# Performance work log

Measured on AMD Instinct MI355X. Metric: run time of the kernel, lower is better.

Reference implementation:

```python
import jax, jax.numpy as jnp
import numpy as np

B, T, M, P, F = 1024, 50, 128, 128, 64  # batch, timesteps, enc_hidden, dec_hidden, feat
BN_EPS = 1e-5


def setup_inputs() -> dict:
    key = jax.random.key(0)
    ks = jax.random.split(key, 20)
    s = 0.05
    inp = {
        "X_encoded": jax.random.normal(ks[0], (B, T, M), jnp.float32),
        "y_prev": jax.random.normal(ks[1], (B, T, F), jnp.float32),
        # attn_layer: Linear(2P+M -> M), Tanh, Linear(M -> 1)
        "attn_w1": jax.random.normal(ks[2], (M, 2 * P + M), jnp.float32) * s,
        "attn_b1": jnp.zeros((M,), jnp.float32),
        "attn_w2": jax.random.normal(ks[3], (1, M), jnp.float32) * s,
        "attn_b2": jnp.zeros((1,), jnp.float32),
        # fc: Linear(M+F -> F) + BatchNorm1d(F) (eval mode, running stats)
        "fc_w": jax.random.normal(ks[4], (F, M + F), jnp.float32) * s,
        "fc_b": jnp.zeros((F,), jnp.float32),
        "bn_gamma": jnp.ones((F,), jnp.float32),
        "bn_beta": jnp.zeros((F,), jnp.float32),
        "bn_mean": jnp.zeros((F,), jnp.float32),
        "bn_var": jnp.ones((F,), jnp.float32),
        # 2-layer LSTM (input F -> hidden P); gate order i,f,g,o as in torch
        "w_ih0": jax.random.normal(ks[5], (4 * P, F), jnp.float32) * s,
        "w_hh0": jax.random.normal(ks[6], (4 * P, P), jnp.float32) * s,
        "b_ih0": jnp.zeros((4 * P,), jnp.float32),
        "b_hh0": jnp.zeros((4 * P,), jnp.float32),
        "w_ih1": jax.random.normal(ks[7], (4 * P, P), jnp.float32) * s,
        "w_hh1": jax.random.normal(ks[8], (4 * P, P), jnp.float32) * s,
        "b_ih1": jnp.zeros((4 * P,), jnp.float32),
        "b_hh1": jnp.zeros((4 * P,), jnp.float32),
        # fc_final: Linear(P+M -> F) + ReLU
        "fcf_w": jax.random.normal(ks[9], (F, P + M), jnp.float32) * s,
        "fcf_b": jnp.zeros((F,), jnp.float32),
    }
    return inp


def _lstm_cell(x, h, c, w_ih, w_hh, b_ih, b_hh):
    g = x @ w_ih.T + b_ih + h @ w_hh.T + b_hh
    i, f, gg, o = jnp.split(g, 4, axis=-1)
    c2 = jax.nn.sigmoid(f) * c + jax.nn.sigmoid(i) * jnp.tanh(gg)
    h2 = jax.nn.sigmoid(o) * jnp.tanh(c2)
    return h2, c2


def reference(X_encoded, y_prev, attn_w1, attn_b1, attn_w2, attn_b2,
              fc_w, fc_b, bn_gamma, bn_beta, bn_mean, bn_var,
              w_ih0, w_hh0, b_ih0, b_hh0, w_ih1, w_hh1, b_ih1, b_hh1,
              fcf_w, fcf_b):
    b, t, m = X_encoded.shape
    p = w_hh0.shape[1]
    # split attn W1 over the concat [d_n[-1]; c_n[-1]; X_encoded]
    w1_d = attn_w1[:, :p]
    w1_c = attn_w1[:, p:2 * p]
    w1_x = attn_w1[:, 2 * p:]
    x_proj = jnp.einsum('btm,nm->btn', X_encoded, w1_x)  # [B,T,M], loop-invariant

    def step(carry, y_t):
        h0, c0, h1, c1, _ = carry
        state_proj = h1 @ w1_d.T + c1 @ w1_c.T + attn_b1          # [B,M]
        score = jnp.tanh(x_proj + state_proj[:, None, :]) @ attn_w2[0] + attn_b2[0]  # [B,T]
        beta = jax.nn.softmax(score, axis=1)
        context = jnp.einsum('bt,btm->bm', beta, X_encoded)        # [B,M]
        z = jnp.concatenate([context, y_t], axis=1) @ fc_w.T + fc_b
        y_tilde = (z - bn_mean) * jax.lax.rsqrt(bn_var + BN_EPS) * bn_gamma + bn_beta
        h0n, c0n = _lstm_cell(y_tilde, h0, c0, w_ih0, w_hh0, b_ih0, b_hh0)
        h1n, c1n = _lstm_cell(h0n, h1, c1, w_ih1, w_hh1, b_ih1, b_hh1)
        return (h0n, c0n, h1n, c1n, context), None

    zeros_p = jnp.zeros((b, p), X_encoded.dtype)
    zeros_m = jnp.zeros((b, m), X_encoded.dtype)
    init = (zeros_p, zeros_p, zeros_p, zeros_p, zeros_m)
    (h0, c0, h1, c1, context), _ = jax.lax.scan(init=init, f=step, xs=jnp.swapaxes(y_prev, 0, 1))
    y_pred = jax.nn.relu(jnp.concatenate([h1, context], axis=1) @ fcf_w.T + fcf_b)
    return y_pred
```

## Files before the change

kernel.cpp:

```cpp
#include <hip/hip_runtime.h>
#include <math.h>

#define TT 50
#define MM 128
#define PP 128
#define FF 64
#define NB 4
#define NTHR 512
#define BN_EPS 1e-5f

typedef unsigned int   u32;
typedef unsigned short u16;
typedef _Float16 f16x8 __attribute__((ext_vector_type(8)));
typedef float    f32x4 __attribute__((ext_vector_type(4)));

#define MFMA16(a, b, c) __builtin_amdgcn_mfma_f32_16x16x32_f16((a), (b), (c), 0, 0, 0)

__device__ __forceinline__ float fsig(float x)  { return 1.0f / (1.0f + __expf(-x)); }
__device__ __forceinline__ float ftanh(float x) { return 1.0f - 2.0f / (__expf(2.0f * x) + 1.0f); }
__device__ __forceinline__ u16 f2h(float x) { _Float16 h = (_Float16)x; u16 r; __builtin_memcpy(&r, &h, 2); return r; }
__device__ __forceinline__ float h2f(u16 u) { _Float16 h; __builtin_memcpy(&h, &u, 2); return (float)h; }

__device__ __forceinline__ void lds_barrier() {
    asm volatile("s_waitcnt lgkmcnt(0)\n\ts_barrier" ::: "memory");
}

__global__ __launch_bounds__(256) void packA_k(const float* __restrict__ w1, u16* __restrict__ dst) {
    int i = blockIdx.x * 256 + threadIdx.x;
    if (i >= 8 * 8 * 64 * 8) return;
    int j = i & 7, l = (i >> 3) & 63, ks = (i >> 9) & 7, tile = i >> 12;
    int row = tile * 16 + (l & 15);
    int k = ks * 32 + ((l >> 4) & 3) * 8 + j;
    dst[i] = f2h(w1[row * 384 + k]);
}
__global__ __launch_bounds__(256) void packE_k(const float* __restrict__ fcw, u16* __restrict__ dst) {
    int i = blockIdx.x * 256 + threadIdx.x;
    if (i >= 4 * 6 * 64 * 8) return;
    int j = i & 7, l = (i >> 3) & 63, r = i >> 9;
    int ks = r % 6, tile = r / 6;
    int row = tile * 16 + (l & 15);
    int k = ks * 32 + ((l >> 4) & 3) * 8 + j;
    dst[i] = f2h(fcw[row * 192 + k]);
}
__global__ __launch_bounds__(256) void packF_k(const float* __restrict__ wih0, const float* __restrict__ whh0,
                                               u16* __restrict__ dst) {
    int i = blockIdx.x * 256 + threadIdx.x;
    if (i >= 8 * 24 * 64 * 8) return;
    int j = i & 7, l = (i >> 3) & 63, rem = i >> 9;
    int wv = rem / 24, t = rem % 24, ks = t >> 2, g = t & 3;
    int row = g * 128 + wv * 16 + (l & 15);
    int k = ks * 32 + ((l >> 4) & 3) * 8 + j;
    float v = (k < 64) ? wih0[row * 64 + k] : whh0[row * 128 + (k - 64)];
    dst[i] = f2h(v);
}
__global__ __launch_bounds__(256) void packG_k(const float* __restrict__ wih1, const float* __restrict__ whh1,
                                               u16* __restrict__ dst) {
    int i = blockIdx.x * 256 + threadIdx.x;
    if (i >= 8 * 32 * 64 * 8) return;
    int j = i & 7, l = (i >> 3) & 63, rem = i >> 9;
    int wv = rem >> 5, t = rem & 31, ks = t >> 2, g = t & 3;
    int row = g * 128 + wv * 16 + (l & 15);
    int k = ks * 32 + ((l >> 4) & 3) * 8 + j;
    float v = (k < 128) ? wih1[row * 128 + k] : whh1[row * 128 + (k - 128)];
    dst[i] = f2h(v);
}

__global__ __launch_bounds__(NTHR, 2) void decoder_kernel(
    const float* __restrict__ X,
    const float* __restrict__ yprev,
    const float* __restrict__ w1,
    const float* __restrict__ b1,
    const float* __restrict__ w2,
    const float* __restrict__ b2,
    const float* __restrict__ fcb,
    const float* __restrict__ bng,
    const float* __restrict__ bnb,
    const float* __restrict__ bnm,
    const float* __restrict__ bnv,
    const float* __restrict__ bih0,
    const float* __restrict__ bhh0,
    const float* __restrict__ bih1,
    const float* __restrict__ bhh1,
    const float* __restrict__ fcfw,
    const float* __restrict__ fcfb,
    const u16* __restrict__ pA,
    const u16* __restrict__ pE,
    const u16* __restrict__ pF,
    const u16* __restrict__ pG,
    float* __restrict__ out)
{
    __shared__ __align__(16) u16   Xh[NB][TT][136];
    __shared__ __align__(16) u16   xph[NB][TT][140];
    __shared__ __align__(16) u16   h0h[2][NB][144];
    __shared__ __align__(16) u16   h1h[2][NB][144];
    __shared__ __align__(16) u16   c1h[NB][144];
    __shared__ __align__(16) u16   ytilh[NB][72];
    __shared__ __align__(16) u16   ctyh[NB][200];
    __shared__ __align__(16) float spf[NB][132];
    __shared__ __align__(16) float c0f[NB][132], c1f[NB][132];
    __shared__ __align__(16) float scs[NB][68];
    __shared__ __align__(16) float b1s[128], w2s[128];
    __shared__ __align__(16) float fck0s[FF], fck1s[FF];
    __shared__ __align__(16) float bsum0s[512], bsum1s[512];

    const int tid = threadIdx.x;
    const int b0 = blockIdx.x * NB;
    const int wv = tid >> 6, l = tid & 63;
    const int kg = (l >> 4) & 3;
    const int c4 = l & 3;
    const int cown = l & 15;

    for (int i4 = tid; i4 < NB * TT * 32; i4 += NTHR) {
        int bb = i4 / (TT * 32);
        int r  = i4 % (TT * 32);
        float4 v = ((const float4*)(X + (size_t)(b0 + bb) * TT * MM))[r];
        uint2 pk;
        pk.x = (u32)f2h(v.x) | ((u32)f2h(v.y) << 16);
        pk.y = (u32)f2h(v.z) | ((u32)f2h(v.w) << 16);
        *(uint2*)&Xh[bb][r >> 5][(r & 31) * 4] = pk;
    }
    for (int i = tid; i < NB * 144; i += NTHR) {
        int bb = i / 144, k = i % 144;
        h0h[0][bb][k] = 0; h0h[1][bb][k] = 0;
        h1h[0][bb][k] = 0; h1h[1][bb][k] = 0;
        c1h[bb][k] = 0;
        if (k < 132) { c0f[bb][k] = 0.f; c1f[bb][k] = 0.f; }
    }
    if (tid < 128) { b1s[tid] = b1[tid]; w2s[tid] = w2[tid]; }
    else if (tid < 192) {
        int f = tid - 128;
        float k1 = rsqrtf(bnv[f] + BN_EPS) * bng[f];
        fck1s[f] = k1;
        fck0s[f] = (fcb[f] - bnm[f]) * k1 + bnb[f];
    }
    bsum0s[tid] = bih0[tid] + bhh0[tid];
    bsum1s[tid] = bih1[tid] + bhh1[tid];

    const int bq = tid >> 7, rr = tid & 127;
    const bool own = rr < 2 * TT;
    const int tq = rr >> 1, qq = rr & 1;
    const float b2v = b2[0];

    if (own) {
        float xf[64];
        #pragma unroll
        for (int n = 0; n < 64; ++n) xf[n] = 0.f;
        const float* Xrow = X + ((size_t)(b0 + bq) * TT + tq) * MM;
        for (int m4 = 0; m4 < 32; ++m4) {
            float4 xv = *(const float4*)(Xrow + m4 * 4);
            #pragma unroll
            for (int n = 0; n < 64; ++n) {
                float4 w = *(const float4*)(w1 + (size_t)(qq * 64 + n) * 384 + 256 + m4 * 4);
                xf[n] += xv.x * w.x + xv.y * w.y + xv.z * w.z + xv.w * w.w;
            }
        }
        #pragma unroll
        for (int j = 0; j < 32; ++j) {
            u32 pk = (u32)f2h(xf[2 * j]) | ((u32)f2h(xf[2 * j + 1]) << 16);
            *(u32*)&xph[bq][tq][qq * 64 + 2 * j] = pk;
        }
    }
    __syncthreads();

    for (int ts = 0; ts < TT; ++ts) {
        const int p = ts & 1;

        {
            f32x4 acc = *(const f32x4*)&b1s[wv * 16 + kg * 4];
            const u16* abase = pA + (size_t)(wv * 8) * 512 + (size_t)l * 8;
            #pragma unroll
            for (int ks = 0; ks < 8; ++ks) {
                f16x8 a = *(const f16x8*)(abase + ks * 512);
                const u16* bp = (ks < 4) ? &h1h[p][c4][ks * 32 + kg * 8]
                                         : &c1h[c4][(ks - 4) * 32 + kg * 8];
                acc = MFMA16(a, *(const f16x8*)bp, acc);
            }
            if (cown < 4) *(f32x4*)&spf[cown][wv * 16 + kg * 4] = acc;
        }
        f16x8 ew[6];
        if (wv < 4) {
            const u16* abase = pE + (size_t)(wv * 6) * 512 + (size_t)l * 8;
            #pragma unroll
            for (int ks = 0; ks < 6; ++ks) ew[ks] = *(const f16x8*)(abase + ks * 512);
        }
        lds_barrier();

        if (own) {
            float acc = 0.f;
            #pragma unroll
            for (int jb = 0; jb < 8; ++jb) {
                int n = qq * 64 + jb * 8;
                uint4 xv  = *(const uint4*)&xph[bq][tq][n];
                f32x4 sp0 = *(const f32x4*)&spf[bq][n];
                f32x4 sp1 = *(const f32x4*)&spf[bq][n + 4];
                f32x4 wv0 = *(const f32x4*)&w2s[n];
                f32x4 wv1 = *(const f32x4*)&w2s[n + 4];
                acc += ftanh(h2f((u16)(xv.x & 0xffffu)) + sp0[0]) * wv0[0];
                acc += ftanh(h2f((u16)(xv.x >> 16))     + sp0[1]) * wv0[1];
                acc += ftanh(h2f((u16)(xv.y & 0xffffu)) + sp0[2]) * wv0[2];
                acc += ftanh(h2f((u16)(xv.y >> 16))     + sp0[3]) * wv0[3];
                acc += ftanh(h2f((u16)(xv.z & 0xffffu)) + sp1[0]) * wv1[0];
                acc += ftanh(h2f((u16)(xv.z >> 16))     + sp1[1]) * wv1[1];
                acc += ftanh(h2f((u16)(xv.w & 0xffffu)) + sp1[2]) * wv1[2];
                acc += ftanh(h2f((u16)(xv.w >> 16))     + sp1[3]) * wv1[3];
            }
            acc += __shfl_xor(acc, 1);
            if (qq == 0) scs[bq][tq] = acc + b2v;
        }
        lds_barrier();

        if (tid < 256) {
            int b = tid >> 6, t = tid & 63;
            float v = (t < TT) ? scs[b][t] : -1e30f;
            float mx = v;
            #pragma unroll
            for (int o = 32; o; o >>= 1) mx = fmaxf(mx, __shfl_xor(mx, o));
            float e = (t < TT) ? __expf(v - mx) : 0.f;
            float s = e;
            #pragma unroll
            for (int o = 32; o; o >>= 1) s += __shfl_xor(s, o);
            if (t < TT) scs[b][t] = e / s;
        } else {
            int i = tid - 256; int bb = i >> 6, f = i & 63;
            ctyh[bb][128 + f] = f2h(yprev[((size_t)(b0 + bb) * TT + ts) * FF + f]);
        }
        lds_barrier();

        f16x8 fw0[8];
        {
            const u16* pw = pF + (size_t)wv * 24 * 512 + (size_t)l * 8;
            #pragma unroll
            for (int q = 0; q < 8; ++q) fw0[q] = *(const f16x8*)(pw + q * 512);
        }
        {
            int bb = tid >> 7, m = tid & 127;
            float acc = 0.f;
            #pragma unroll 10
            for (int t = 0; t < TT; ++t) acc += scs[bb][t] * h2f(Xh[bb][t][m]);
            ctyh[bb][m] = f2h(acc);
        }
        lds_barrier();

        if (wv < 4) {
            f32x4 acc = {0.f, 0.f, 0.f, 0.f};
            #pragma unroll
            for (int ks = 0; ks < 6; ++ks) {
                f16x8 b = *(const f16x8*)&ctyh[c4][ks * 32 + kg * 8];
                acc = MFMA16(ew[ks], b, acc);
            }
            if (cown < 4) {
                int row = wv * 16 + kg * 4;
                f32x4 k1 = *(const f32x4*)&fck1s[row];
                f32x4 k0 = *(const f32x4*)&fck0s[row];
                #pragma unroll
                for (int r = 0; r < 4; ++r)
                    ytilh[cown][row + r] = f2h(acc[r] * k1[r] + k0[r]);
            }
        }
        lds_barrier();

        f16x8 gw0[8];
        {
            const u16* pw = pF + (size_t)wv * 24 * 512 + (size_t)l * 8;
            f32x4 a0 = *(const f32x4*)&bsum0s[0 * 128 + wv * 16 + kg * 4];
            f32x4 a1 = *(const f32x4*)&bsum0s[1 * 128 + wv * 16 + kg * 4];
            f32x4 a2 = *(const f32x4*)&bsum0s[2 * 128 + wv * 16 + kg * 4];
            f32x4 a3 = *(const f32x4*)&bsum0s[3 * 128 + wv * 16 + kg * 4];
            #pragma unroll
            for (int ks = 0; ks < 2; ++ks) {
                f16x8 b = *(const f16x8*)&ytilh[c4][ks * 32 + kg * 8];
                a0 = MFMA16(fw0[ks * 4 + 0], b, a0);
                a1 = MFMA16(fw0[ks * 4 + 1], b, a1);
                a2 = MFMA16(fw0[ks * 4 + 2], b, a2);
                a3 = MFMA16(fw0[ks * 4 + 3], b, a3);
            }
            #pragma unroll
            for (int ks = 2; ks < 6; ++ks) {
                f16x8 b = *(const f16x8*)&h0h[p][c4][(ks - 2) * 32 + kg * 8];
                a0 = MFMA16(*(const f16x8*)(pw + (ks * 4 + 0) * 512), b, a0);
                a1 = MFMA16(*(const f16x8*)(pw + (ks * 4 + 1) * 512), b, a1);
                a2 = MFMA16(*(const f16x8*)(pw + (ks * 4 + 2) * 512), b, a2);
                a3 = MFMA16(*(const f16x8*)(pw + (ks * 4 + 3) * 512), b, a3);
            }
            {
                const u16* pwg = pG + (size_t)wv * 32 * 512 + (size_t)l * 8;
                #pragma unroll
                for (int q = 0; q < 8; ++q) gw0[q] = *(const f16x8*)(pwg + q * 512);
            }
            if (cown < 4) {
                int cb = wv * 16 + kg * 4;
                u32 lo, hi;
                {
                    float gi = fsig(a0[0]), gF = fsig(a1[0]), gG = ftanh(a2[0]), gO = fsig(a3[0]);
                    float cn = gF * c0f[cown][cb + 0] + gi * gG;
                    c0f[cown][cb + 0] = cn;
                    lo = (u32)f2h(gO * ftanh(cn));
                }
                {
                    float gi = fsig(a0[1]), gF = fsig(a1[1]), gG = ftanh(a2[1]), gO = fsig(a3[1]);
                    float cn = gF * c0f[cown][cb + 1] + gi * gG;
                    c0f[cown][cb + 1] = cn;
                    lo |= (u32)f2h(gO * ftanh(cn)) << 16;
                }
                {
                    float gi = fsig(a0[2]), gF = fsig(a1[2]), gG = ftanh(a2[2]), gO = fsig(a3[2]);
                    float cn = gF * c0f[cown][cb + 2] + gi * gG;
                    c0f[cown][cb + 2] = cn;
                    hi = (u32)f2h(gO * ftanh(cn));
                }
                {
                    float gi = fsig(a0[3]), gF = fsig(a1[3]), gG = ftanh(a2[3]), gO = fsig(a3[3]);
                    float cn = gF * c0f[cown][cb + 3] + gi * gG;
                    c0f[cown][cb + 3] = cn;
                    hi |= (u32)f2h(gO * ftanh(cn)) << 16;
                }
                uint2 pk; pk.x = lo; pk.y = hi;
                *(uint2*)&h0h[p ^ 1][cown][cb] = pk;
            }
        }
        lds_barrier();

        {
            const u16* pw = pG + (size_t)wv * 32 * 512 + (size_t)l * 8;
            f32x4 a0 = *(const f32x4*)&bsum1s[0 * 128 + wv * 16 + kg * 4];
            f32x4 a1 = *(const f32x4*)&bsum1s[1 * 128 + wv * 16 + kg * 4];
            f32x4 a2 = *(const f32x4*)&bsum1s[2 * 128 + wv * 16 + kg * 4];
            f32x4 a3 = *(const f32x4*)&bsum1s[3 * 128 + wv * 16 + kg * 4];
            #pragma unroll
            for (int ks = 0; ks < 2; ++ks) {
                f16x8 b = *(const f16x8*)&h0h[p ^ 1][c4][ks * 32 + kg * 8];
                a0 = MFMA16(gw0[ks * 4 + 0], b, a0);
                a1 = MFMA16(gw0[ks * 4 + 1], b, a1);
                a2 = MFMA16(gw0[ks * 4 + 2], b, a2);
                a3 = MFMA16(gw0[ks * 4 + 3], b, a3);
            }
            #pragma unroll
            for (int ks = 2; ks < 8; ++ks) {
                const u16* bp = (ks < 4) ? &h0h[p ^ 1][c4][ks * 32 + kg * 8]
                                         : &h1h[p][c4][(ks - 4) * 32 + kg * 8];
                f16x8 b = *(const f16x8*)bp;
                a0 = MFMA16(*(const f16x8*)(pw + (ks * 4 + 0) * 512), b, a0);
                a1 = MFMA16(*(const f16x8*)(pw + (ks * 4 + 1) * 512), b, a1);
                a2 = MFMA16(*(const f16x8*)(pw + (ks * 4 + 2) * 512), b, a2);
                a3 = MFMA16(*(const f16x8*)(pw + (ks * 4 + 3) * 512), b, a3);
            }
            if (cown < 4) {
                int cb = wv * 16 + kg * 4;
                u32 lo, hi, clo, chi;
                {
                    float gi = fsig(a0[0]), gF = fsig(a1[0]), gG = ftanh(a2[0]), gO = fsig(a3[0]);
                    float cn = gF * c1f[cown][cb + 0] + gi * gG;
                    c1f[cown][cb + 0] = cn;
                    clo = (u32)f2h(cn);
                    lo  = (u32)f2h(gO * ftanh(cn));
                }
                {
                    float gi = fsig(a0[1]), gF = fsig(a1[1]), gG = ftanh(a2[1]), gO = fsig(a3[1]);
                    float cn = gF * c1f[cown][cb + 1] + gi * gG;
                    c1f[cown][cb + 1] = cn;
                    clo |= (u32)f2h(cn) << 16;
                    lo  |= (u32)f2h(gO * ftanh(cn)) << 16;
                }
                {
                    float gi = fsig(a0[2]), gF = fsig(a1[2]), gG = ftanh(a2[2]), gO = fsig(a3[2]);
                    float cn = gF * c1f[cown][cb + 2] + gi * gG;
                    c1f[cown][cb + 2] = cn;
                    chi = (u32)f2h(cn);
                    hi  = (u32)f2h(gO * ftanh(cn));
                }
                {
                    float gi = fsig(a0[3]), gF = fsig(a1[3]), gG = ftanh(a2[3]), gO = fsig(a3[3]);
                    float cn = gF * c1f[cown][cb + 3] + gi * gG;
                    c1f[cown][cb + 3] = cn;
                    chi |= (u32)f2h(cn) << 16;
                    hi  |= (u32)f2h(gO * ftanh(cn)) << 16;
                }
                uint2 pk; pk.x = lo; pk.y = hi;
                *(uint2*)&h1h[p ^ 1][cown][cb] = pk;
                uint2 ck; ck.x = clo; ck.y = chi;
                *(uint2*)&c1h[cown][cb] = ck;
            }
        }
        lds_barrier();
    }

    if (tid < 256) {
        int f = tid >> 2, bb = tid & 3;
        const float* wr = fcfw + (size_t)f * 256;
        float acc = fcfb[f];
        #pragma unroll 4
        for (int k4 = 0; k4 < 32; ++k4) {
            float4 w = *(const float4*)(wr + k4 * 4);
            acc += w.x * h2f(h1h[0][bb][k4 * 4 + 0]) + w.y * h2f(h1h[0][bb][k4 * 4 + 1])
                 + w.z * h2f(h1h[0][bb][k4 * 4 + 2]) + w.w * h2f(h1h[0][bb][k4 * 4 + 3]);
        }
        #pragma unroll 4
        for (int k4 = 0; k4 < 32; ++k4) {
            float4 w = *(const float4*)(wr + 128 + k4 * 4);
            acc += w.x * h2f(ctyh[bb][k4 * 4 + 0]) + w.y * h2f(ctyh[bb][k4 * 4 + 1])
                 + w.z * h2f(ctyh[bb][k4 * 4 + 2]) + w.w * h2f(ctyh[bb][k4 * 4 + 3]);
        }
        out[(size_t)(b0 + bb) * FF + f] = fmaxf(acc, 0.f);
    }
}

extern "C" void kernel_launch(void* const* d_in, const int* in_sizes, int n_in,
                              void* d_out, int out_size, void* d_ws, size_t ws_size,
                              hipStream_t stream) {
    (void)in_sizes; (void)n_in; (void)out_size; (void)ws_size;
    const float* X    = (const float*)d_in[0];
    const float* yp   = (const float*)d_in[1];
    const float* w1   = (const float*)d_in[2];
    const float* b1   = (const float*)d_in[3];
    const float* w2   = (const float*)d_in[4];
    const float* b2   = (const float*)d_in[5];
    const float* fcw  = (const float*)d_in[6];
    const float* fcb  = (const float*)d_in[7];
    const float* bng  = (const float*)d_in[8];
    const float* bnb  = (const float*)d_in[9];
    const float* bnm  = (const float*)d_in[10];
    const float* bnv  = (const float*)d_in[11];
    const float* wih0 = (const float*)d_in[12];
    const float* whh0 = (const float*)d_in[13];
    const float* bih0 = (const float*)d_in[14];
    const float* bhh0 = (const float*)d_in[15];
    const float* wih1 = (const float*)d_in[16];
    const float* whh1 = (const float*)d_in[17];
    const float* bih1 = (const float*)d_in[18];
    const float* bhh1 = (const float*)d_in[19];
    const float* fcfw = (const float*)d_in[20];
    const float* fcfb = (const float*)d_in[21];
    float* out = (float*)d_out;

    u16* pA = (u16*)d_ws;
    u16* pE = pA + 32768;
    u16* pF = pE + 12288;
    u16* pG = pF + 98304;

    packA_k<<<dim3(32768 / 256), dim3(256), 0, stream>>>(w1, pA);
    packE_k<<<dim3(12288 / 256), dim3(256), 0, stream>>>(fcw, pE);
    packF_k<<<dim3(98304 / 256), dim3(256), 0, stream>>>(wih0, whh0, pF);
    packG_k<<<dim3(131072 / 256), dim3(256), 0, stream>>>(wih1, whh1, pG);

    decoder_kernel<<<dim3(1024 / NB), dim3(NTHR), 0, stream>>>(
        X, yp, w1, b1, w2, b2, fcb, bng, bnb, bnm, bnv,
        bih0, bhh0, bih1, bhh1, fcfw, fcfb, pA, pE, pF, pG, out);
}
```

Baseline: 843.4 us.

## Transpose encoder tile in LDS for vectorized context reduction and prefetch more layer-1 weights

Stores the per-batch encoder tile transposed (m-major, t contiguous, padded to 52 with zeros) so the attention-weighted context sum reads four fp16 values and four scores per LDS load instead of one scalar pair per timestep. Padding entries of both the tile and the score buffer are zeroed so the 13x4 unrolled loop stays correct. It also prefetches a second bank of layer-1 LSTM weights into registers during the layer-0 gate math, hiding more global-load latency behind the recurrence. The cost is more VGPR pressure and a strided, bank-conflict-prone scatter when building the transposed tile at setup.

```diff
diff --git a/kernel.cpp b/kernel.cpp
--- a/kernel.cpp
+++ b/kernel.cpp
@@ -89,7 +89,7 @@
     const u16* __restrict__ pG,
     float* __restrict__ out)
 {
-    __shared__ __align__(16) u16   Xh[NB][TT][136];
+    __shared__ __align__(16) u16   XhT[NB][MM][60];
     __shared__ __align__(16) u16   xph[NB][TT][140];
     __shared__ __align__(16) u16   h0h[2][NB][144];
     __shared__ __align__(16) u16   h1h[2][NB][144];
@@ -113,12 +113,18 @@
     for (int i4 = tid; i4 < NB * TT * 32; i4 += NTHR) {
         int bb = i4 / (TT * 32);
         int r  = i4 % (TT * 32);
+        int t = r >> 5, m4 = (r & 31) * 4;
         float4 v = ((const float4*)(X + (size_t)(b0 + bb) * TT * MM))[r];
-        uint2 pk;
-        pk.x = (u32)f2h(v.x) | ((u32)f2h(v.y) << 16);
-        pk.y = (u32)f2h(v.z) | ((u32)f2h(v.w) << 16);
-        *(uint2*)&Xh[bb][r >> 5][(r & 31) * 4] = pk;
-    }
+        XhT[bb][m4 + 0][t] = f2h(v.x);
+        XhT[bb][m4 + 1][t] = f2h(v.y);
+        XhT[bb][m4 + 2][t] = f2h(v.z);
+        XhT[bb][m4 + 3][t] = f2h(v.w);
+    }
+    {
+        int bb = tid >> 7, m = tid & 127;
+        XhT[bb][m][50] = 0; XhT[bb][m][51] = 0;
+    }
+    if (tid < NB * 8) scs[tid >> 3][50 + (tid & 7)] = 0.f;
     for (int i = tid; i < NB * 144; i += NTHR) {
         int bb = i / 144, k = i % 144;
         h0h[0][bb][k] = 0; h0h[1][bb][k] = 0;
@@ -235,8 +241,15 @@
         {
             int bb = tid >> 7, m = tid & 127;
             float acc = 0.f;
-            #pragma unroll 10
-            for (int t = 0; t < TT; ++t) acc += scs[bb][t] * h2f(Xh[bb][t][m]);
+            #pragma unroll
+            for (int t4 = 0; t4 < 13; ++t4) {
+                uint2 xv = *(const uint2*)&XhT[bb][m][t4 * 4];
+                f32x4 sc = *(const f32x4*)&scs[bb][t4 * 4];
+                acc += sc[0] * h2f((u16)(xv.x & 0xffffu));
+                acc += sc[1] * h2f((u16)(xv.x >> 16));
+                acc += sc[2] * h2f((u16)(xv.y & 0xffffu));
+                acc += sc[3] * h2f((u16)(xv.y >> 16));
+            }
             ctyh[bb][m] = f2h(acc);
         }
         lds_barrier();
@@ -259,7 +272,7 @@
         }
         lds_barrier();
 
-        f16x8 gw0[8];
+        f16x8 gw0[8], gw1[8];
         {
             const u16* pw = pF + (size_t)wv * 24 * 512 + (size_t)l * 8;
             f32x4 a0 = *(const f32x4*)&bsum0s[0 * 128 + wv * 16 + kg * 4];
@@ -286,6 +299,8 @@
                 const u16* pwg = pG + (size_t)wv * 32 * 512 + (size_t)l * 8;
                 #pragma unroll
                 for (int q = 0; q < 8; ++q) gw0[q] = *(const f16x8*)(pwg + q * 512);
+                #pragma unroll
+                for (int q = 0; q < 8; ++q) gw1[q] = *(const f16x8*)(pwg + (8 + q) * 512);
             }
             if (cown < 4) {
                 int cb = wv * 16 + kg * 4;
@@ -335,10 +350,16 @@
                 a3 = MFMA16(gw0[ks * 4 + 3], b, a3);
             }
             #pragma unroll
-            for (int ks = 2; ks < 8; ++ks) {
-                const u16* bp = (ks < 4) ? &h0h[p ^ 1][c4][ks * 32 + kg * 8]
-                                         : &h1h[p][c4][(ks - 4) * 32 + kg * 8];
-                f16x8 b = *(const f16x8*)bp;
+            for (int ks = 2; ks < 4; ++ks) {
+                f16x8 b = *(const f16x8*)&h0h[p ^ 1][c4][ks * 32 + kg * 8];
+                a0 = MFMA16(gw1[(ks - 2) * 4 + 0], b, a0);
+                a1 = MFMA16(gw1[(ks - 2) * 4 + 1], b, a1);
+                a2 = MFMA16(gw1[(ks - 2) * 4 + 2], b, a2);
+                a3 = MFMA16(gw1[(ks - 2) * 4 + 3], b, a3);
+            }
+            #pragma unroll
+            for (int ks = 4; ks < 8; ++ks) {
+                f16x8 b = *(const f16x8*)&h1h[p][c4][(ks - 4) * 32 + kg * 8];
                 a0 = MFMA16(*(const f16x8*)(pw + (ks * 4 + 0) * 512), b, a0);
                 a1 = MFMA16(*(const f16x8*)(pw + (ks * 4 + 1) * 512), b, a1);
                 a2 = MFMA16(*(const f16x8*)(pw + (ks * 4 + 2) * 512), b, a2);
```

Result: slower. 949.0 us (+12.5%).

## Hoist recurrent h@W_hh MFMA partial sums to step start, off critical path

Applied to the files above, without the earlier changes.

The recurrent parts of both LSTM layers' gate matmuls (h0 against W_hh0 and h1 against W_hh1) depend only on the previous timestep's state. They are now computed at the start of each timestep, alongside the attention state projection, and kept in accumulator registers. After the context and y_tilde are ready, only the input-dependent MFMAs remain, which shortens the serial dependency chain between barriers. The cost is 32 extra live accumulator VGPRs across the attention and softmax phases, which could raise register pressure or cause spills.

```diff
diff --git a/kernel.cpp b/kernel.cpp
--- a/kernel.cpp
+++ b/kernel.cpp
@@ -165,6 +165,8 @@
     for (int ts = 0; ts < TT; ++ts) {
         const int p = ts & 1;
 
+        f32x4 facc0, facc1, facc2, facc3;
+        f32x4 gacc0, gacc1, gacc2, gacc3;
         {
             f32x4 acc = *(const f32x4*)&b1s[wv * 16 + kg * 4];
             const u16* abase = pA + (size_t)(wv * 8) * 512 + (size_t)l * 8;
@@ -176,6 +178,36 @@
                 acc = MFMA16(a, *(const f16x8*)bp, acc);
             }
             if (cown < 4) *(f32x4*)&spf[cown][wv * 16 + kg * 4] = acc;
+        }
+        {
+            const u16* pwf = pF + (size_t)wv * 24 * 512 + (size_t)l * 8;
+            facc0 = *(const f32x4*)&bsum0s[0 * 128 + wv * 16 + kg * 4];
+            facc1 = *(const f32x4*)&bsum0s[1 * 128 + wv * 16 + kg * 4];
+            facc2 = *(const f32x4*)&bsum0s[2 * 128 + wv * 16 + kg * 4];
+            facc3 = *(const f32x4*)&bsum0s[3 * 128 + wv * 16 + kg * 4];
+            #pragma unroll
+            for (int ks = 2; ks < 6; ++ks) {
+                f16x8 b = *(const f16x8*)&h0h[p][c4][(ks - 2) * 32 + kg * 8];
+                facc0 = MFMA16(*(const f16x8*)(pwf + (ks * 4 + 0) * 512), b, facc0);
+                facc1 = MFMA16(*(const f16x8*)(pwf + (ks * 4 + 1) * 512), b, facc1);
+                facc2 = MFMA16(*(const f16x8*)(pwf + (ks * 4 + 2) * 512), b, facc2);
+                facc3 = MFMA16(*(const f16x8*)(pwf + (ks * 4 + 3) * 512), b, facc3);
+            }
+        }
+        {
+            const u16* pwg = pG + (size_t)wv * 32 * 512 + (size_t)l * 8;
+            gacc0 = *(const f32x4*)&bsum1s[0 * 128 + wv * 16 + kg * 4];
+            gacc1 = *(const f32x4*)&bsum1s[1 * 128 + wv * 16 + kg * 4];
+            gacc2 = *(const f32x4*)&bsum1s[2 * 128 + wv * 16 + kg * 4];
+            gacc3 = *(const f32x4*)&bsum1s[3 * 128 + wv * 16 + kg * 4];
+            #pragma unroll
+            for (int ks = 4; ks < 8; ++ks) {
+                f16x8 b = *(const f16x8*)&h1h[p][c4][(ks - 4) * 32 + kg * 8];
+                gacc0 = MFMA16(*(const f16x8*)(pwg + (ks * 4 + 0) * 512), b, gacc0);
+                gacc1 = MFMA16(*(const f16x8*)(pwg + (ks * 4 + 1) * 512), b, gacc1);
+                gacc2 = MFMA16(*(const f16x8*)(pwg + (ks * 4 + 2) * 512), b, gacc2);
+                gacc3 = MFMA16(*(const f16x8*)(pwg + (ks * 4 + 3) * 512), b, gacc3);
+            }
         }
         f16x8 ew[6];
         if (wv < 4) {
@@ -226,12 +258,6 @@
         }
         lds_barrier();
 
-        f16x8 fw0[8];
-        {
-            const u16* pw = pF + (size_t)wv * 24 * 512 + (size_t)l * 8;
-            #pragma unroll
-            for (int q = 0; q < 8; ++q) fw0[q] = *(const f16x8*)(pw + q * 512);
-        }
         {
             int bb = tid >> 7, m = tid & 127;
             float acc = 0.f;
@@ -241,6 +267,12 @@
         }
         lds_barrier();
 
+        f16x8 fw0[8];
+        {
+            const u16* pwf = pF + (size_t)wv * 24 * 512 + (size_t)l * 8;
+            #pragma unroll
+            for (int q = 0; q < 8; ++q) fw0[q] = *(const f16x8*)(pwf + q * 512);
+        }
         if (wv < 4) {
             f32x4 acc = {0.f, 0.f, 0.f, 0.f};
             #pragma unroll
@@ -259,13 +291,8 @@
         }
         lds_barrier();
 
-        f16x8 gw0[8];
-        {
-            const u16* pw = pF + (size_t)wv * 24 * 512 + (size_t)l * 8;
-            f32x4 a0 = *(const f32x4*)&bsum0s[0 * 128 + wv * 16 + kg * 4];
-            f32x4 a1 = *(const f32x4*)&bsum0s[1 * 128 + wv * 16 + kg * 4];
-            f32x4 a2 = *(const f32x4*)&bsum0s[2 * 128 + wv * 16 + kg * 4];
-            f32x4 a3 = *(const f32x4*)&bsum0s[3 * 128 + wv * 16 + kg * 4];
+        {
+            f32x4 a0 = facc0, a1 = facc1, a2 = facc2, a3 = facc3;
             #pragma unroll
             for (int ks = 0; ks < 2; ++ks) {
                 f16x8 b = *(const f16x8*)&ytilh[c4][ks * 32 + kg * 8];
@@ -274,19 +301,6 @@
                 a2 = MFMA16(fw0[ks * 4 + 2], b, a2);
                 a3 = MFMA16(fw0[ks * 4 + 3], b, a3);
             }
-            #pragma unroll
-            for (int ks = 2; ks < 6; ++ks) {
-                f16x8 b = *(const f16x8*)&h0h[p][c4][(ks - 2) * 32 + kg * 8];
-                a0 = MFMA16(*(const f16x8*)(pw + (ks * 4 + 0) * 512), b, a0);
-                a1 = MFMA16(*(const f16x8*)(pw + (ks * 4 + 1) * 512), b, a1);
-                a2 = MFMA16(*(const f16x8*)(pw + (ks * 4 + 2) * 512), b, a2);
-                a3 = MFMA16(*(const f16x8*)(pw + (ks * 4 + 3) * 512), b, a3);
-            }
-            {
-                const u16* pwg = pG + (size_t)wv * 32 * 512 + (size_t)l * 8;
-                #pragma unroll
-                for (int q = 0; q < 8; ++q) gw0[q] = *(const f16x8*)(pwg + q * 512);
-            }
             if (cown < 4) {
                 int cb = wv * 16 + kg * 4;
                 u32 lo, hi;
@@ -322,23 +336,10 @@
 
         {
             const u16* pw = pG + (size_t)wv * 32 * 512 + (size_t)l * 8;
-            f32x4 a0 = *(const f32x4*)&bsum1s[0 * 128 + wv * 16 + kg * 4];
-            f32x4 a1 = *(const f32x4*)&bsum1s[1 * 128 + wv * 16 + kg * 4];
-            f32x4 a2 = *(const f32x4*)&bsum1s[2 * 128 + wv * 16 + kg * 4];
-            f32x4 a3 = *(const f32x4*)&bsum1s[3 * 128 + wv * 16 + kg * 4];
-            #pragma unroll
-            for (int ks = 0; ks < 2; ++ks) {
+            f32x4 a0 = gacc0, a1 = gacc1, a2 = gacc2, a3 = gacc3;
+            #pragma unroll
+            for (int ks = 0; ks < 4; ++ks) {
                 f16x8 b = *(const f16x8*)&h0h[p ^ 1][c4][ks * 32 + kg * 8];
-                a0 = MFMA16(gw0[ks * 4 + 0], b, a0);
-                a1 = MFMA16(gw0[ks * 4 + 1], b, a1);
-                a2 = MFMA16(gw0[ks * 4 + 2], b, a2);
-                a3 = MFMA16(gw0[ks * 4 + 3], b, a3);
-            }
-            #pragma unroll
-            for (int ks = 2; ks < 8; ++ks) {
-                const u16* bp = (ks < 4) ? &h0h[p ^ 1][c4][ks * 32 + kg * 8]
-                                         : &h1h[p][c4][(ks - 4) * 32 + kg * 8];
-                f16x8 b = *(const f16x8*)bp;
                 a0 = MFMA16(*(const f16x8*)(pw + (ks * 4 + 0) * 512), b, a0);
                 a1 = MFMA16(*(const f16x8*)(pw + (ks * 4 + 1) * 512), b, a1);
                 a2 = MFMA16(*(const f16x8*)(pw + (ks * 4 + 2) * 512), b, a2);
```

Result: slower. 1.353 ms (+60.5%).
